# Optimization experiments

Hardware: AMD Instinct MI355X
Metric: run time of the kernel (lower is better)

Reference implementation:

```python
import jax, jax.numpy as jnp
from jax import lax
import numpy as np

NB_HEAD = 8
D_MODEL = 64
KERNEL = 3


def setup_inputs() -> dict:
    key = jax.random.key(0)
    k1, k2, k3, k4, k5 = jax.random.split(key, 5)
    B, N, T, D = 16, 1024, 24, D_MODEL
    value = jax.random.normal(k1, (B, N, T, D), dtype=jnp.float32)
    # Conv2d(d_model, d_model, (1, kernel_size)) weights (OIHW) + bias
    fan_in = D * 1 * KERNEL
    bound = 1.0 / np.sqrt(fan_in)
    W_conv = jax.random.uniform(k2, (D, D, 1, KERNEL), jnp.float32, -bound, bound)
    b_conv = jax.random.uniform(k3, (D,), jnp.float32, -bound, bound)
    # Linear(d_model, d_model): W (out, in), bias (out,)
    lb = 1.0 / np.sqrt(D)
    W_lin = jax.random.uniform(k4, (D, D), jnp.float32, -lb, lb)
    b_lin = jax.random.uniform(k5, (D,), jnp.float32, -lb, lb)
    return {"value": value, "W_conv": W_conv, "b_conv": b_conv,
            "W_lin": W_lin, "b_lin": b_lin}


def reference(value, W_conv, b_conv, W_lin, b_lin):
    B, N, T, D = value.shape
    h = NB_HEAD
    d_k = D // h
    pad = (KERNEL - 1) // 2
    # conv1D_aware_temporal_context1 on value.permute(0,3,1,2): (B, D, N, T)
    x = jnp.transpose(value, (0, 3, 1, 2))
    x = lax.conv_general_dilated(
        x, W_conv, window_strides=(1, 1), padding=[(0, 0), (pad, pad)],
        dimension_numbers=("NCHW", "OIHW", "NCHW"))
    x = x + b_conv[None, :, None, None]
    # view(B, h, d_k, N, T).permute(0,3,1,4,2) -> (B, N, h, T, d_k)
    v = jnp.transpose(x.reshape(B, h, d_k, N, T), (0, 3, 1, 4, 2))
    # relation_matrix_h is the tridiagonal all-ones band -> out[t] = v[t-1]+v[t]+v[t+1]
    vp = jnp.pad(v, ((0, 0), (0, 0), (0, 0), (1, 1), (0, 0)))
    v = vp[..., :-2, :] + vp[..., 1:-1, :] + vp[..., 2:, :]
    # transpose(2,3) then merge heads: (B, N, T, h*d_k)
    v = jnp.transpose(v, (0, 1, 3, 2, 4)).reshape(B, N, T, h * d_k)
    # linear_output1 + relu
    out = jax.nn.relu(jnp.einsum("bntd,od->bnto", v, W_lin) + b_lin)
    return out
```

## Files before the change

kernel.cpp:

```cpp
#include <hip/hip_runtime.h>
#include <hip/hip_bf16.h>


typedef __attribute__((ext_vector_type(8))) short short8;
typedef __attribute__((ext_vector_type(8))) __bf16 bf16x8;
typedef __attribute__((ext_vector_type(4))) float f4;

#define R_ROWS 8
#define GROUPS 4
#define VP_STRIDE 72
#define V_ROW_ELEMS (26 * VP_STRIDE)

__device__ __forceinline__ unsigned short f2bfu(float f) {
    return __bfloat16_as_ushort(__float2bfloat16(f));
}

__global__ void prep_kernel(const float* __restrict__ Wconv,
                            const float* __restrict__ bconv,
                            const float* __restrict__ Wlin,
                            const float* __restrict__ blin,
                            __hip_bfloat16* __restrict__ wbig,
                            float* __restrict__ biasC,
                            float* __restrict__ blinF) {
    __shared__ float Wl[4096];
    const int tid = threadIdx.x;
    for (int c = tid; c < 4096; c += 256) Wl[c] = Wlin[c];
    __syncthreads();
    int idx = blockIdx.x * 256 + tid;
    if (idx < 64 * 192) {
        int o = idx / 192;
        int j = idx - o * 192;
        int k = j >> 6;
        int i = j & 63;
        float acc = 0.0f;
        for (int c = 0; c < 64; ++c)
            acc += Wl[o * 64 + c] * Wconv[c * 192 + i * 3 + k];
        wbig[o * 192 + j] = __float2bfloat16(acc);
    } else if (idx < 64 * 192 + 64) {
        int o = idx - 64 * 192;
        float acc = 0.0f;
        for (int c = 0; c < 64; ++c)
            acc += Wl[o * 64 + c] * bconv[c];
        biasC[o] = acc;
    } else if (idx < 64 * 192 + 128) {
        int o = idx - (64 * 192 + 64);
        blinF[o] = blin[o];
    }
}

__global__ __launch_bounds__(256, 2) void fused_kernel(
    const float* __restrict__ value,
    const __hip_bfloat16* __restrict__ wbig,
    const float* __restrict__ biasC,
    const float* __restrict__ blinF,
    float* __restrict__ out) {
    __shared__ __align__(16) short Vlds[2][R_ROWS * V_ROW_ELEMS];

    const int tid = threadIdx.x;
    const int wave = tid >> 6;
    const int lane = tid & 63;
    const int lane15 = lane & 15;
    const int quad = lane >> 4;
    const long block_row0 = (long)blockIdx.x * (R_ROWS * GROUPS);

    int goff[12], loff[12];
    #pragma unroll
    for (int j = 0; j < 12; ++j) {
        int c4 = tid + 256 * j;
        int r = c4 / 384;
        int rem = c4 - r * 384;
        int t = rem >> 4;
        int d4 = (rem & 15) << 2;
        goff[j] = r * 1536 + t * 64 + d4;
        loff[j] = r * V_ROW_ELEMS + (t + 1) * VP_STRIDE + d4;
    }
    if (tid < 128) {
        int r = tid >> 4;
        int which = (tid >> 3) & 1;
        int d8 = (tid & 7) << 3;
        uint4 z; z.x = 0; z.y = 0; z.z = 0; z.w = 0;
        *(uint4*)(&Vlds[0][0] + r * V_ROW_ELEMS + which * (25 * VP_STRIDE) + d8) = z;
        *(uint4*)(&Vlds[1][0] + r * V_ROW_ELEMS + which * (25 * VP_STRIDE) + d8) = z;
    }

    const short* wsrc = (const short*)wbig;
    const int k0 = quad * 8;
    bf16x8 breg[6];
    #pragma unroll
    for (int ks = 0; ks < 6; ++ks)
        breg[ks] = __builtin_bit_cast(bf16x8,
            *(const short8*)(wsrc + (wave * 16 + lane15) * 192 + ks * 32 + k0));

    f4 pre[12];
    {
        const float* vb = value + block_row0 * 1536;
        #pragma unroll
        for (int j = 0; j < 12; ++j)
            pre[j] = *(const f4*)(vb + goff[j]);
        #pragma unroll
        for (int j = 0; j < 12; ++j) {
            ushort4 u;
            u.x = f2bfu(pre[j].x); u.y = f2bfu(pre[j].y);
            u.z = f2bfu(pre[j].z); u.w = f2bfu(pre[j].w);
            *(ushort4*)(&Vlds[0][0] + loff[j]) = u;
        }
    }
    __syncthreads();

    int aoff[12];
    #pragma unroll
    for (int mt = 0; mt < 12; ++mt) {
        int m = mt * 16 + lane15;
        int r = m / 24;
        int s = m - r * 24;
        aoff[mt] = r * V_ROW_ELEMS + s * VP_STRIDE;
    }

    const int o = wave * 16 + lane15;
    const float bc = biasC[o];
    const float bl = blinF[o];
    const float b3 = 3.0f * bc + bl;
    const float b2 = 2.0f * bc + bl;
    const int srcP = (lane + 48) & 63;
    const int srcN = (lane + 16) & 63;

    int p = 0;
    for (int g = 0; g < GROUPS; ++g) {
        if (g + 1 < GROUPS) {
            const float* vb = value + (block_row0 + (long)(g + 1) * R_ROWS) * 1536;
            #pragma unroll
            for (int j = 0; j < 12; ++j)
                pre[j] = *(const f4*)(vb + goff[j]);
        }

        const short* Vcur = &Vlds[p][0];
        f4 acc[12];
        #pragma unroll
        for (int mt = 0; mt < 12; ++mt) {
            f4 zz = {0.f, 0.f, 0.f, 0.f};
            acc[mt] = zz;
        }
        #pragma unroll
        for (int ks = 0; ks < 6; ++ks) {
            int k = ks * 32 + k0;
            int ka = ((k >> 6) * VP_STRIDE) + (k & 63);
            #pragma unroll
            for (int mt = 0; mt < 12; ++mt) {
                bf16x8 a = __builtin_bit_cast(bf16x8,
                    *(const short8*)(Vcur + aoff[mt] + ka));
                acc[mt] = __builtin_amdgcn_mfma_f32_16x16x32_bf16(
                    a, breg[ks], acc[mt], 0, 0, 0);
            }
        }

        const long grow0 = block_row0 + (long)g * R_ROWS;
        #pragma unroll
        for (int mt = 0; mt < 12; ++mt) {
            const int mtp = (mt > 0) ? mt - 1 : 0;
            const int mtn = (mt < 11) ? mt + 1 : 11;
            float pin = __shfl(acc[mt][3], srcP, 64);
            float pxr = __shfl(acc[mtp][3], srcP, 64);
            float nin = __shfl(acc[mt][0], srcN, 64);
            float nxr = __shfl(acc[mtn][0], srcN, 64);
            float prev0 = (quad == 0) ? pxr : pin;
            float next3 = (quad == 3) ? nxr : nin;
            #pragma unroll
            for (int i = 0; i < 4; ++i) {
                int rowq = mt * 16 + quad * 4 + i;
                int rr = rowq / 24;
                int t = rowq - rr * 24;
                float s = acc[mt][i];
                float prev = (i > 0) ? acc[mt][i - 1] : prev0;
                float next = (i < 3) ? acc[mt][i + 1] : next3;
                if (t > 0)  s += prev;
                if (t < 23) s += next;
                float r = fmaxf(s + ((t == 0 || t == 23) ? b2 : b3), 0.0f);
                out[((grow0 + rr) * 24 + t) * 64 + o] = r;
            }
        }

        if (g + 1 < GROUPS) {
            short* Vnxt = &Vlds[p ^ 1][0];
            #pragma unroll
            for (int j = 0; j < 12; ++j) {
                ushort4 u;
                u.x = f2bfu(pre[j].x); u.y = f2bfu(pre[j].y);
                u.z = f2bfu(pre[j].z); u.w = f2bfu(pre[j].w);
                *(ushort4*)(Vnxt + loff[j]) = u;
            }
            __syncthreads();
        }
        p ^= 1;
    }
}

extern "C" void kernel_launch(void* const* d_in, const int* in_sizes, int n_in,
                              void* d_out, int out_size, void* d_ws, size_t ws_size,
                              hipStream_t stream) {
    const float* value = (const float*)d_in[0];
    const float* Wconv = (const float*)d_in[1];
    const float* bconv = (const float*)d_in[2];
    const float* Wlin  = (const float*)d_in[3];
    const float* blin  = (const float*)d_in[4];
    float* out = (float*)d_out;

    __hip_bfloat16* wbig = (__hip_bfloat16*)d_ws;
    float* biasC = (float*)((char*)d_ws + 24576);
    float* blinF = (float*)((char*)d_ws + 24832);

    prep_kernel<<<49, 256, 0, stream>>>(Wconv, bconv, Wlin, blin, wbig, biasC, blinF);
    fused_kernel<<<512, 256, 0, stream>>>(value, wbig, biasC, blinF, out);
}
```

Before: 200.1 us.

## Replace per-block software pipeline with one tile per block and more blocks

Drops the four-group double-buffered loop so each block handles a single 8-row tile with one LDS buffer, launching four times as many blocks. Launch bounds are raised to allow four resident blocks per CU. The intent is to hide global-memory latency through occupancy and many in-flight blocks rather than through explicit prefetch. The trade-off is repeated weight-register loads and LDS padding setup per block, plus tighter register limits that could cause spills.

```diff
diff --git a/kernel.cpp b/kernel.cpp
--- a/kernel.cpp
+++ b/kernel.cpp
@@ -7,7 +7,6 @@
 typedef __attribute__((ext_vector_type(4))) float f4;
 
 #define R_ROWS 8
-#define GROUPS 4
 #define VP_STRIDE 72
 #define V_ROW_ELEMS (26 * VP_STRIDE)
 
@@ -48,40 +47,20 @@
     }
 }
 
-__global__ __launch_bounds__(256, 2) void fused_kernel(
+__global__ __launch_bounds__(256, 4) void fused_kernel(
     const float* __restrict__ value,
     const __hip_bfloat16* __restrict__ wbig,
     const float* __restrict__ biasC,
     const float* __restrict__ blinF,
     float* __restrict__ out) {
-    __shared__ __align__(16) short Vlds[2][R_ROWS * V_ROW_ELEMS];
+    __shared__ __align__(16) short Vlds[R_ROWS * V_ROW_ELEMS];
 
     const int tid = threadIdx.x;
     const int wave = tid >> 6;
     const int lane = tid & 63;
     const int lane15 = lane & 15;
     const int quad = lane >> 4;
-    const long block_row0 = (long)blockIdx.x * (R_ROWS * GROUPS);
-
-    int goff[12], loff[12];
-    #pragma unroll
-    for (int j = 0; j < 12; ++j) {
-        int c4 = tid + 256 * j;
-        int r = c4 / 384;
-        int rem = c4 - r * 384;
-        int t = rem >> 4;
-        int d4 = (rem & 15) << 2;
-        goff[j] = r * 1536 + t * 64 + d4;
-        loff[j] = r * V_ROW_ELEMS + (t + 1) * VP_STRIDE + d4;
-    }
-    if (tid < 128) {
-        int r = tid >> 4;
-        int which = (tid >> 3) & 1;
-        int d8 = (tid & 7) << 3;
-        uint4 z; z.x = 0; z.y = 0; z.z = 0; z.w = 0;
-        *(uint4*)(&Vlds[0][0] + r * V_ROW_ELEMS + which * (25 * VP_STRIDE) + d8) = z;
-        *(uint4*)(&Vlds[1][0] + r * V_ROW_ELEMS + which * (25 * VP_STRIDE) + d8) = z;
-    }
+    const long base_row = (long)blockIdx.x * R_ROWS;
 
     const short* wsrc = (const short*)wbig;
     const int k0 = quad * 8;
@@ -92,18 +71,33 @@
             *(const short8*)(wsrc + (wave * 16 + lane15) * 192 + ks * 32 + k0));
 
     f4 pre[12];
+    int loff[12];
     {
-        const float* vb = value + block_row0 * 1536;
-        #pragma unroll
-        for (int j = 0; j < 12; ++j)
-            pre[j] = *(const f4*)(vb + goff[j]);
+        const float* vb = value + base_row * 1536;
         #pragma unroll
         for (int j = 0; j < 12; ++j) {
-            ushort4 u;
-            u.x = f2bfu(pre[j].x); u.y = f2bfu(pre[j].y);
-            u.z = f2bfu(pre[j].z); u.w = f2bfu(pre[j].w);
-            *(ushort4*)(&Vlds[0][0] + loff[j]) = u;
+            int c4 = tid + 256 * j;
+            int r = c4 / 384;
+            int rem = c4 - r * 384;
+            int t = rem >> 4;
+            int d4 = (rem & 15) << 2;
+            pre[j] = *(const f4*)(vb + r * 1536 + t * 64 + d4);
+            loff[j] = r * V_ROW_ELEMS + (t + 1) * VP_STRIDE + d4;
         }
+    }
+    if (tid < 128) {
+        int r = tid >> 4;
+        int which = (tid >> 3) & 1;
+        int d8 = (tid & 7) << 3;
+        uint4 z; z.x = 0; z.y = 0; z.z = 0; z.w = 0;
+        *(uint4*)(Vlds + r * V_ROW_ELEMS + which * (25 * VP_STRIDE) + d8) = z;
+    }
+    #pragma unroll
+    for (int j = 0; j < 12; ++j) {
+        ushort4 u;
+        u.x = f2bfu(pre[j].x); u.y = f2bfu(pre[j].y);
+        u.z = f2bfu(pre[j].z); u.w = f2bfu(pre[j].w);
+        *(ushort4*)(Vlds + loff[j]) = u;
     }
     __syncthreads();
 
@@ -115,6 +109,24 @@
         int s = m - r * 24;
         aoff[mt] = r * V_ROW_ELEMS + s * VP_STRIDE;
     }
+    f4 acc[12];
+    #pragma unroll
+    for (int mt = 0; mt < 12; ++mt) {
+        f4 zz = {0.f, 0.f, 0.f, 0.f};
+        acc[mt] = zz;
+    }
+    #pragma unroll
+    for (int ks = 0; ks < 6; ++ks) {
+        int k = ks * 32 + k0;
+        int ka = ((k >> 6) * VP_STRIDE) + (k & 63);
+        #pragma unroll
+        for (int mt = 0; mt < 12; ++mt) {
+            bf16x8 a = __builtin_bit_cast(bf16x8,
+                *(const short8*)(Vlds + aoff[mt] + ka));
+            acc[mt] = __builtin_amdgcn_mfma_f32_16x16x32_bf16(
+                a, breg[ks], acc[mt], 0, 0, 0);
+        }
+    }
 
     const int o = wave * 16 + lane15;
     const float bc = biasC[o];
@@ -123,74 +135,29 @@
     const float b2 = 2.0f * bc + bl;
     const int srcP = (lane + 48) & 63;
     const int srcN = (lane + 16) & 63;
-
-    int p = 0;
-    for (int g = 0; g < GROUPS; ++g) {
-        if (g + 1 < GROUPS) {
-            const float* vb = value + (block_row0 + (long)(g + 1) * R_ROWS) * 1536;
-            #pragma unroll
-            for (int j = 0; j < 12; ++j)
-                pre[j] = *(const f4*)(vb + goff[j]);
+    #pragma unroll
+    for (int mt = 0; mt < 12; ++mt) {
+        const int mtp = (mt > 0) ? mt - 1 : 0;
+        const int mtn = (mt < 11) ? mt + 1 : 11;
+        float pin = __shfl(acc[mt][3], srcP, 64);
+        float pxr = __shfl(acc[mtp][3], srcP, 64);
+        float nin = __shfl(acc[mt][0], srcN, 64);
+        float nxr = __shfl(acc[mtn][0], srcN, 64);
+        float prev0 = (quad == 0) ? pxr : pin;
+        float next3 = (quad == 3) ? nxr : nin;
+        #pragma unroll
+        for (int i = 0; i < 4; ++i) {
+            int rowq = mt * 16 + quad * 4 + i;
+            int rr = rowq / 24;
+            int t = rowq - rr * 24;
+            float s = acc[mt][i];
+            float prev = (i > 0) ? acc[mt][i - 1] : prev0;
+            float next = (i < 3) ? acc[mt][i + 1] : next3;
+            if (t > 0)  s += prev;
+            if (t < 23) s += next;
+            float r = fmaxf(s + ((t == 0 || t == 23) ? b2 : b3), 0.0f);
+            out[((base_row + rr) * 24 + t) * 64 + o] = r;
         }
-
-        const short* Vcur = &Vlds[p][0];
-        f4 acc[12];
-        #pragma unroll
-        for (int mt = 0; mt < 12; ++mt) {
-            f4 zz = {0.f, 0.f, 0.f, 0.f};
-            acc[mt] = zz;
-        }
-        #pragma unroll
-        for (int ks = 0; ks < 6; ++ks) {
-            int k = ks * 32 + k0;
-            int ka = ((k >> 6) * VP_STRIDE) + (k & 63);
-            #pragma unroll
-            for (int mt = 0; mt < 12; ++mt) {
-                bf16x8 a = __builtin_bit_cast(bf16x8,
-                    *(const short8*)(Vcur + aoff[mt] + ka));
-                acc[mt] = __builtin_amdgcn_mfma_f32_16x16x32_bf16(
-                    a, breg[ks], acc[mt], 0, 0, 0);
-            }
-        }
-
-        const long grow0 = block_row0 + (long)g * R_ROWS;
-        #pragma unroll
-        for (int mt = 0; mt < 12; ++mt) {
-            const int mtp = (mt > 0) ? mt - 1 : 0;
-            const int mtn = (mt < 11) ? mt + 1 : 11;
-            float pin = __shfl(acc[mt][3], srcP, 64);
-            float pxr = __shfl(acc[mtp][3], srcP, 64);
-            float nin = __shfl(acc[mt][0], srcN, 64);
-            float nxr = __shfl(acc[mtn][0], srcN, 64);
-            float prev0 = (quad == 0) ? pxr : pin;
-            float next3 = (quad == 3) ? nxr : nin;
-            #pragma unroll
-            for (int i = 0; i < 4; ++i) {
-                int rowq = mt * 16 + quad * 4 + i;
-                int rr = rowq / 24;
-                int t = rowq - rr * 24;
-                float s = acc[mt][i];
-                float prev = (i > 0) ? acc[mt][i - 1] : prev0;
-                float next = (i < 3) ? acc[mt][i + 1] : next3;
-                if (t > 0)  s += prev;
-                if (t < 23) s += next;
-                float r = fmaxf(s + ((t == 0 || t == 23) ? b2 : b3), 0.0f);
-                out[((grow0 + rr) * 24 + t) * 64 + o] = r;
-            }
-        }
-
-        if (g + 1 < GROUPS) {
-            short* Vnxt = &Vlds[p ^ 1][0];
-            #pragma unroll
-            for (int j = 0; j < 12; ++j) {
-                ushort4 u;
-                u.x = f2bfu(pre[j].x); u.y = f2bfu(pre[j].y);
-                u.z = f2bfu(pre[j].z); u.w = f2bfu(pre[j].w);
-                *(ushort4*)(Vnxt + loff[j]) = u;
-            }
-            __syncthreads();
-        }
-        p ^= 1;
     }
 }
 
@@ -209,5 +176,5 @@
     float* blinF = (float*)((char*)d_ws + 24832);
 
     prep_kernel<<<49, 256, 0, stream>>>(Wconv, bconv, Wlin, blin, wbig, biasC, blinF);
-    fused_kernel<<<512, 256, 0, stream>>>(value, wbig, biasC, blinF, out);
+    fused_kernel<<<2048, 256, 0, stream>>>(value, wbig, biasC, blinF, out);
 }
```

After: 193.6 us. 3.2% less time.
